# Kernel tuning notes

Hardware: AMD Instinct MI355X
Metric: run time of the kernel (lower is better)

The kernel has to match this reference:

```python
import jax, jax.numpy as jnp
import numpy as np

N_ATOMS = 20
LS_PER_ATOM = [0, 0, 1, 1, 2]   # two s, two p, one d shell per atom
N_PRIM = 8
N_COORDS = 131072


def cart_angulars(l):
    return np.array([[lx, ly, l - lx - ly]
                     for lx in range(l, -1, -1)
                     for ly in range(l - lx, -1, -1)], dtype=np.float32)


def fact2(n):
    n = int(n)
    if n <= 0:
        return 1.0
    r = 1.0
    while n > 1:
        r *= n
        n -= 2
    return r


# ---- static shell bookkeeping (grouped by angular momentum l) ----
SHELL_ATOM = np.array([a for a in range(N_ATOMS) for _ in LS_PER_ATOM])
SHELL_L = np.array([l for _ in range(N_ATOMS) for l in LS_PER_ATOM])
N_SHELLS = len(SHELL_L)
UNIQUE_LS = sorted(set(LS_PER_ATOM))

GROUPS = {}
for l in UNIQUE_LS:
    idx = np.where(SHELL_L == l)[0]
    ls = cart_angulars(l)  # [ncart, 3]
    anorms = 1.0 / np.sqrt(np.array(
        [np.prod([fact2(2 * int(e) - 1) for e in row]) for row in ls],
        dtype=np.float64))
    GROUPS[l] = (idx, ls, anorms.astype(np.float32))

NAO_CART = sum(len(GROUPS[l][1]) * len(GROUPS[l][0]) for l in UNIQUE_LS)  # 280
NAO_SPH = sum((2 * l + 1) * len(GROUPS[l][0]) for l in UNIQUE_LS)          # 260


def setup_inputs() -> dict:
    key = jax.random.key(0)
    k1, k2, k3, k4, k5, k6 = jax.random.split(key, 6)
    coords = jax.random.normal(k1, (N_COORDS, 3), dtype=jnp.float32) * 2.0
    centers = jax.random.normal(k2, (N_ATOMS, 3), dtype=jnp.float32) * 3.0
    # Gaussian exponents must be positive
    zetas = jax.random.uniform(k3, (N_SHELLS, N_PRIM), dtype=jnp.float32,
                               minval=0.2, maxval=3.0)
    coeffs = jax.random.normal(k4, (N_SHELLS, N_PRIM), dtype=jnp.float32)
    normalization = jax.random.uniform(k5, (NAO_CART,), dtype=jnp.float32,
                                       minval=0.5, maxval=1.5)
    cart2sph = jax.random.normal(k6, (NAO_CART, NAO_SPH), dtype=jnp.float32) * 0.3
    return {"coords": coords, "centers": centers, "zetas": zetas,
            "coeffs": coeffs, "normalization": normalization,
            "cart2sph": cart2sph}


def reference(coords, centers, zetas, coeffs, normalization, cart2sph):
    """Batched GTOBasis.eval_ao: [N,3] -> [N, nao_sph]."""
    n = coords.shape[0]
    pieces = []
    for l in UNIQUE_LS:
        idx, ls, anorms = GROUPS[l]
        c = centers[SHELL_ATOM[idx]]                 # [S, 3]
        rs = coords[:, None, :] - c[None]            # [N, S, 3]
        rs2 = jnp.sum(rs * rs, axis=-1)              # [N, S]
        # cartesian angular part: prod over xyz of rs**l_component
        ang = jnp.prod(rs[:, :, None, :] ** jnp.asarray(ls)[None, None],
                       axis=-1)                      # [N, S, ncart]
        ex = jnp.exp(-zetas[idx][None] * rs2[:, :, None])  # [N, S, nprim]
        rad = jnp.sum(coeffs[idx][None] * ex, axis=-1)     # [N, S]
        phis = jnp.asarray(anorms) * ang * rad[:, :, None]  # [N, S, ncart]
        pieces.append(phis.reshape(n, -1))
    aos = jnp.concatenate(pieces, axis=-1) * normalization  # [N, nao_cart]
    return jnp.dot(aos, cart2sph)                           # [N, nao_sph]
```

## Files before the change

kernel.cpp:

```cpp
#include <hip/hip_runtime.h>

typedef unsigned int uint;
typedef unsigned short ushort;
typedef __attribute__((ext_vector_type(8))) short short8;
typedef __attribute__((ext_vector_type(4))) float f32x4;
typedef __attribute__((ext_vector_type(2))) uint uint2v;

#define NSH   100
#define NPRIM 8
#define NAOC  280
#define NAOS  260
#define NATOM 20
#define KP    288
#define NKB   9
#define MT    32
#define NCOLP 272
#define BCH   (32 * NCOLP)
#define RSQRT3 0.57735026918962576f
#define LOG2E  1.4426950408889634f
#define EPS   276

#define O_RAD   0
#define O_AH    12800
#define O_AL    16896
#define O_ZETA  20992
#define O_COEF  24192
#define O_CEN   27392
#define O_CX    27712
#define O_CY    27840
#define O_CZ    27968
#define O_NORMF 28096
#define O_META  29248
#define POOLSZ  (MT * EPS * 4)

__device__ __forceinline__ ushort bf16_rne(float x) {
    uint u = __float_as_uint(x);
    return (ushort)((u + 0x7FFFu + ((u >> 16) & 1u)) >> 16);
}
__device__ __forceinline__ float bf16_to_f(ushort h) {
    return __uint_as_float(((uint)h) << 16);
}
__device__ __forceinline__ uint cvt_pk_bf16(float a, float b) {
    uint r;
    asm("v_cvt_pk_bf16_f32 %0, %1, %2" : "=v"(r) : "v"(a), "v"(b));
    return r;
}

__device__ __forceinline__ int calc_meta(int k, float& anorm) {
    int shell = 0, atom = 0, s1 = 0, s2 = 0;
    anorm = 1.0f;
    if (k < 40) {
        atom = k >> 1; shell = 5 * atom + (k & 1);
    } else if (k < 160) {
        int i = k - 40; int ip = i / 3; int c = i - 3 * ip;
        atom = ip >> 1; shell = 5 * atom + 2 + (ip & 1); s1 = 1 + c;
    } else if (k < NAOC) {
        int i = k - 160; atom = i / 6; shell = 5 * atom + 4; int c = i - 6 * atom;
        if      (c == 0) { s1 = 1; s2 = 1; }
        else if (c == 1) { s1 = 1; s2 = 2; }
        else if (c == 2) { s1 = 1; s2 = 3; }
        else if (c == 3) { s1 = 2; s2 = 2; }
        else if (c == 4) { s1 = 2; s2 = 3; }
        else             { s1 = 3; s2 = 3; }
        if (c == 0 || c == 3 || c == 5) anorm = RSQRT3;
    }
    return shell | (atom << 7) | (s1 << 12) | (s2 << 14);
}

__global__ void prep_b(const float* __restrict__ c2s, const float* __restrict__ norm,
                       ushort* __restrict__ wsHi, ushort* __restrict__ wsLo,
                       int* __restrict__ wsMeta, float* __restrict__ wsNorm) {
    if (blockIdx.x == 0) {
        for (int k = threadIdx.x; k < KP; k += 256) {
            float an;
            int m = calc_meta(k, an);
            wsMeta[k] = m;
            wsNorm[k] = (k < NAOC ? norm[k] : 0.0f) * an;
        }
    }
    int id = blockIdx.x * 256 + threadIdx.x;
    if (id >= KP * NCOLP) return;
    int k = id / NCOLP, col = id % NCOLP;
    float v = (k < NAOC && col < NAOS) ? c2s[k * NAOS + col] : 0.0f;
    ushort hi = bf16_rne(v);
    ushort lo = bf16_rne(v - bf16_to_f(hi));
    int off = (k >> 5) * BCH +
              (((col >> 4) * 4 + ((k & 31) >> 3)) * 16 + (col & 15)) * 8 + (k & 7);
    wsHi[off] = hi;
    wsLo[off] = lo;
}

template <bool USEWS>
__global__ __launch_bounds__(256, 4) void gto_mfma(
    const float* __restrict__ coords, const float* __restrict__ centers,
    const float* __restrict__ zetas, const float* __restrict__ coeffs,
    const float* __restrict__ norm, const float* __restrict__ c2s,
    const ushort* __restrict__ wsHi, const ushort* __restrict__ wsLo,
    const int* __restrict__ wsMeta, const float* __restrict__ wsNorm,
    float* __restrict__ out, int n)
{
    __shared__ __align__(16) char smem[POOLSZ];
    float*  sRad  = (float*)(smem + O_RAD);
    float*  sZeta = (float*)(smem + O_ZETA);
    float*  sCoef = (float*)(smem + O_COEF);
    float4* sCen4 = (float4*)(smem + O_CEN);
    float*  sCx   = (float*)(smem + O_CX);
    float*  sCy   = (float*)(smem + O_CY);
    float*  sCz   = (float*)(smem + O_CZ);
    float*  sNormF= (float*)(smem + O_NORMF);
    int*    sMeta = (int*)(smem + O_META);

    const int t = threadIdx.x, lane = t & 63, w = t >> 6;
    const int lr = lane & 15, lg4 = lane >> 4;
    const int P0 = blockIdx.x * MT;

    for (int i = t; i < NSH * NPRIM; i += 256) {
        sZeta[i] = zetas[i] * LOG2E;
        sCoef[i] = coeffs[i];
    }
    if (t < NATOM)
        sCen4[t] = make_float4(centers[3 * t], centers[3 * t + 1], centers[3 * t + 2], 0.0f);
    if (t < MT * 3) {
        int gi = P0 * 3 + t;
        float v = (gi < 3 * n) ? coords[gi] : 0.0f;
        int p = t / 3, c = t - 3 * (t / 3);
        if (c == 0) sCx[p] = v; else if (c == 1) sCy[p] = v; else sCz[p] = v;
    }
    if (USEWS) {
        for (int i = t; i < KP; i += 256) { sMeta[i] = wsMeta[i]; sNormF[i] = wsNorm[i]; }
    } else {
        for (int k = t; k < KP; k += 256) {
            float an;
            sMeta[k] = calc_meta(k, an);
            sNormF[k] = (k < NAOC ? norm[k] : 0.0f) * an;
        }
    }
    __syncthreads();

    #pragma unroll 1
    for (int it = 0; it < (NSH * MT + 255) / 256; ++it) {
        int id = it * 256 + t;
        if (id < NSH * MT) {
            int s = id >> 5, p = id & 31;
            int a = s / 5;
            float4 ca = sCen4[a];
            float dx = sCx[p] - ca.x;
            float dy = sCy[p] - ca.y;
            float dz = sCz[p] - ca.z;
            float r2 = dx * dx + dy * dy + dz * dz;
            float4 z0 = *(const float4*)&sZeta[s * NPRIM];
            float4 z1 = *(const float4*)&sZeta[s * NPRIM + 4];
            float4 c0 = *(const float4*)&sCoef[s * NPRIM];
            float4 c1 = *(const float4*)&sCoef[s * NPRIM + 4];
            float rad = c0.x * __builtin_amdgcn_exp2f(-z0.x * r2);
            rad += c0.y * __builtin_amdgcn_exp2f(-z0.y * r2);
            rad += c0.z * __builtin_amdgcn_exp2f(-z0.z * r2);
            rad += c0.w * __builtin_amdgcn_exp2f(-z0.w * r2);
            rad += c1.x * __builtin_amdgcn_exp2f(-z1.x * r2);
            rad += c1.y * __builtin_amdgcn_exp2f(-z1.y * r2);
            rad += c1.z * __builtin_amdgcn_exp2f(-z1.z * r2);
            rad += c1.w * __builtin_amdgcn_exp2f(-z1.w * r2);
            sRad[s * MT + p] = rad;
        }
    }

    const int pA = t & 31, kg = t >> 5;
    auto buildA = [&](int kb2) {
        const float cxp = sCx[pA], cyp = sCy[pA], czp = sCz[pA];
        const int k0 = kb2 * 32 + kg * 4;
        int4   m4  = *(const int4*)&sMeta[k0];
        float4 nf4 = *(const float4*)&sNormF[k0];
        float v[4];
        const int   mk[4] = {m4.x, m4.y, m4.z, m4.w};
        const float nf[4] = {nf4.x, nf4.y, nf4.z, nf4.w};
        #pragma unroll
        for (int j = 0; j < 4; ++j) {
            int meta = mk[j];
            int s = meta & 127, a = (meta >> 7) & 31;
            int s1 = (meta >> 12) & 3, s2 = (meta >> 14) & 3;
            float4 ca = sCen4[a];
            float dx = cxp - ca.x, dy = cyp - ca.y, dz = czp - ca.z;
            float m1 = (s1 == 0) ? 1.0f : ((s1 == 1) ? dx : ((s1 == 2) ? dy : dz));
            float m2 = (s2 == 0) ? 1.0f : ((s2 == 1) ? dx : ((s2 == 2) ? dy : dz));
            v[j] = sRad[s * MT + pA] * (m1 * m2) * nf[j];
        }
        uint h01 = cvt_pk_bf16(v[0], v[1]);
        uint h23 = cvt_pk_bf16(v[2], v[3]);
        float r0 = v[0] - __uint_as_float(h01 << 16);
        float r1 = v[1] - __uint_as_float(h01 & 0xffff0000u);
        float r2 = v[2] - __uint_as_float(h23 << 16);
        float r3 = v[3] - __uint_as_float(h23 & 0xffff0000u);
        uint l01 = cvt_pk_bf16(r0, r1);
        uint l23 = cvt_pk_bf16(r2, r3);
        const int boff = (kb2 & 1) * 2048 + ((kg >> 1) * 512 + pA * 16 + (kg & 1) * 8);
        *(uint2v*)(smem + O_AH + boff) = (uint2v){h01, h23};
        *(uint2v*)(smem + O_AL + boff) = (uint2v){l01, l23};
    };

    __syncthreads();
    buildA(0);

    f32x4 acc[5][2];
    #pragma unroll
    for (int i = 0; i < 5; ++i)
        #pragma unroll
        for (int mt = 0; mt < 2; ++mt)
            acc[i][mt] = (f32x4){0.0f, 0.0f, 0.0f, 0.0f};

    for (int kb = 0; kb < NKB; ++kb) {
        __syncthreads();

        short8 aH[2], aL[2];
        #pragma unroll
        for (int mt = 0; mt < 2; ++mt) {
            int off = (kb & 1) * 2048 + (lg4 * 32 + mt * 16 + lr) * 16;
            aH[mt] = *(const short8*)(smem + O_AH + off);
            aL[mt] = *(const short8*)(smem + O_AL + off);
        }

        if (kb + 1 < NKB) buildA(kb + 1);

        #pragma unroll
        for (int i = 0; i < 5; ++i) {
            if (i < 4 || w == 0) {
                int nt = (i == 4) ? 16 : (w * 4 + i);
                short8 bh, bl;
                if (USEWS) {
                    bh = *(const short8*)(wsHi + (size_t)kb * BCH + (nt * 64 + lane) * 8);
                    bl = *(const short8*)(wsLo + (size_t)kb * BCH + (nt * 64 + lane) * 8);
                } else {
                    #pragma unroll
                    for (int j = 0; j < 8; ++j) {
                        int k = kb * 32 + lg4 * 8 + j;
                        int col = nt * 16 + lr;
                        float v = (k < NAOC && col < NAOS) ? c2s[k * NAOS + col] : 0.0f;
                        ushort hi = bf16_rne(v);
                        bh[j] = (short)hi;
                        bl[j] = (short)bf16_rne(v - bf16_to_f(hi));
                    }
                }
                #pragma unroll
                for (int mt = 0; mt < 2; ++mt)
                    acc[i][mt] = __builtin_amdgcn_mfma_f32_16x16x32_bf16(aH[mt], bh, acc[i][mt], 0, 0, 0);
                #pragma unroll
                for (int mt = 0; mt < 2; ++mt)
                    acc[i][mt] = __builtin_amdgcn_mfma_f32_16x16x32_bf16(aH[mt], bl, acc[i][mt], 0, 0, 0);
                #pragma unroll
                for (int mt = 0; mt < 2; ++mt)
                    acc[i][mt] = __builtin_amdgcn_mfma_f32_16x16x32_bf16(aL[mt], bh, acc[i][mt], 0, 0, 0);
            }
        }
    }

    __syncthreads();
    float* ep = (float*)smem;
    #pragma unroll
    for (int i = 0; i < 5; ++i) {
        if (i < 4 || w == 0) {
            int nt = (i == 4) ? 16 : (w * 4 + i);
            int col = nt * 16 + lr;
            #pragma unroll
            for (int mt = 0; mt < 2; ++mt)
                #pragma unroll
                for (int r = 0; r < 4; ++r)
                    ep[(mt * 16 + lg4 * 4 + r) * EPS + col] = acc[i][mt][r];
        }
    }
    __syncthreads();

    for (int row = w; row < MT; row += 4) {
        int P = P0 + row;
        if (P < n)
            *(float4*)&out[(size_t)P * NAOS + lane * 4] = *(const float4*)&ep[row * EPS + lane * 4];
    }
    if (w == 1 && lane < MT) {
        int P = P0 + lane;
        if (P < n)
            *(float4*)&out[(size_t)P * NAOS + 256] = *(const float4*)&ep[lane * EPS + 256];
    }
}

extern "C" void kernel_launch(void* const* d_in, const int* in_sizes, int n_in,
                              void* d_out, int out_size, void* d_ws, size_t ws_size,
                              hipStream_t stream) {
    const float* coords  = (const float*)d_in[0];
    const float* centers = (const float*)d_in[1];
    const float* zetas   = (const float*)d_in[2];
    const float* coeffs  = (const float*)d_in[3];
    const float* norm    = (const float*)d_in[4];
    const float* c2s     = (const float*)d_in[5];
    float* out = (float*)d_out;
    int n = in_sizes[0] / 3;
    int grid = (n + MT - 1) / MT;

    ushort* wsHi = (ushort*)d_ws;
    ushort* wsLo = wsHi + (size_t)KP * NCOLP;
    int*    wsMeta = (int*)(wsLo + (size_t)KP * NCOLP);
    float*  wsNorm = (float*)(wsMeta + KP);
    const size_t WS_NEED = (size_t)2 * KP * NCOLP * sizeof(ushort) + KP * 8;

    if (ws_size >= WS_NEED) {
        prep_b<<<(KP * NCOLP + 255) / 256, 256, 0, stream>>>(c2s, norm, wsHi, wsLo, wsMeta, wsNorm);
        gto_mfma<true><<<grid, 256, 0, stream>>>(coords, centers, zetas, coeffs, norm, c2s,
                                                 wsHi, wsLo, wsMeta, wsNorm, out, n);
    } else {
        gto_mfma<false><<<grid, 256, 0, stream>>>(coords, centers, zetas, coeffs, norm, c2s,
                                                  nullptr, nullptr, nullptr, nullptr, out, n);
    }
}
```

Measured before the change: 105.6 us.

## Build MFMA A fragments in registers instead of double-buffered shared memory

After: 155.1 us. 46.9% more time.

```diff
diff --git a/kernel.cpp b/kernel.cpp
--- a/kernel.cpp
+++ b/kernel.cpp
@@ -4,7 +4,6 @@
 typedef unsigned short ushort;
 typedef __attribute__((ext_vector_type(8))) short short8;
 typedef __attribute__((ext_vector_type(4))) float f32x4;
-typedef __attribute__((ext_vector_type(2))) uint uint2v;
 
 #define NSH   100
 #define NPRIM 8
@@ -19,18 +18,17 @@
 #define RSQRT3 0.57735026918962576f
 #define LOG2E  1.4426950408889634f
 #define EPS   276
+#define RSTRIDE 33
 
 #define O_RAD   0
-#define O_AH    12800
-#define O_AL    16896
-#define O_ZETA  20992
-#define O_COEF  24192
-#define O_CEN   27392
-#define O_CX    27712
-#define O_CY    27840
-#define O_CZ    27968
-#define O_NORMF 28096
-#define O_META  29248
+#define O_ZETA  13200
+#define O_COEF  16400
+#define O_CEN   19600
+#define O_CX    19920
+#define O_CY    20048
+#define O_CZ    20176
+#define O_NORMF 20304
+#define O_META  21456
 #define POOLSZ  (MT * EPS * 4)
 
 __device__ __forceinline__ ushort bf16_rne(float x) {
@@ -160,45 +158,13 @@
             rad += c1.y * __builtin_amdgcn_exp2f(-z1.y * r2);
             rad += c1.z * __builtin_amdgcn_exp2f(-z1.z * r2);
             rad += c1.w * __builtin_amdgcn_exp2f(-z1.w * r2);
-            sRad[s * MT + p] = rad;
-        }
-    }
-
-    const int pA = t & 31, kg = t >> 5;
-    auto buildA = [&](int kb2) {
-        const float cxp = sCx[pA], cyp = sCy[pA], czp = sCz[pA];
-        const int k0 = kb2 * 32 + kg * 4;
-        int4   m4  = *(const int4*)&sMeta[k0];
-        float4 nf4 = *(const float4*)&sNormF[k0];
-        float v[4];
-        const int   mk[4] = {m4.x, m4.y, m4.z, m4.w};
-        const float nf[4] = {nf4.x, nf4.y, nf4.z, nf4.w};
-        #pragma unroll
-        for (int j = 0; j < 4; ++j) {
-            int meta = mk[j];
-            int s = meta & 127, a = (meta >> 7) & 31;
-            int s1 = (meta >> 12) & 3, s2 = (meta >> 14) & 3;
-            float4 ca = sCen4[a];
-            float dx = cxp - ca.x, dy = cyp - ca.y, dz = czp - ca.z;
-            float m1 = (s1 == 0) ? 1.0f : ((s1 == 1) ? dx : ((s1 == 2) ? dy : dz));
-            float m2 = (s2 == 0) ? 1.0f : ((s2 == 1) ? dx : ((s2 == 2) ? dy : dz));
-            v[j] = sRad[s * MT + pA] * (m1 * m2) * nf[j];
-        }
-        uint h01 = cvt_pk_bf16(v[0], v[1]);
-        uint h23 = cvt_pk_bf16(v[2], v[3]);
-        float r0 = v[0] - __uint_as_float(h01 << 16);
-        float r1 = v[1] - __uint_as_float(h01 & 0xffff0000u);
-        float r2 = v[2] - __uint_as_float(h23 << 16);
-        float r3 = v[3] - __uint_as_float(h23 & 0xffff0000u);
-        uint l01 = cvt_pk_bf16(r0, r1);
-        uint l23 = cvt_pk_bf16(r2, r3);
-        const int boff = (kb2 & 1) * 2048 + ((kg >> 1) * 512 + pA * 16 + (kg & 1) * 8);
-        *(uint2v*)(smem + O_AH + boff) = (uint2v){h01, h23};
-        *(uint2v*)(smem + O_AL + boff) = (uint2v){l01, l23};
-    };
-
+            sRad[s * RSTRIDE + p] = rad;
+        }
+    }
     __syncthreads();
-    buildA(0);
+
+    const float cx0 = sCx[lr],      cy0 = sCy[lr],      cz0 = sCz[lr];
+    const float cx1 = sCx[16 + lr], cy1 = sCy[16 + lr], cz1 = sCz[16 + lr];
 
     f32x4 acc[5][2];
     #pragma unroll
@@ -207,18 +173,50 @@
         for (int mt = 0; mt < 2; ++mt)
             acc[i][mt] = (f32x4){0.0f, 0.0f, 0.0f, 0.0f};
 
+    union U4 { uint u[4]; short8 s; };
+
+    #pragma unroll 1
     for (int kb = 0; kb < NKB; ++kb) {
-        __syncthreads();
+        const int k0 = kb * 32 + lg4 * 8;
+        int4   m4a = *(const int4*)&sMeta[k0];
+        int4   m4b = *(const int4*)&sMeta[k0 + 4];
+        float4 n4a = *(const float4*)&sNormF[k0];
+        float4 n4b = *(const float4*)&sNormF[k0 + 4];
+        const int   mk[8] = {m4a.x, m4a.y, m4a.z, m4a.w, m4b.x, m4b.y, m4b.z, m4b.w};
+        const float nf[8] = {n4a.x, n4a.y, n4a.z, n4a.w, n4b.x, n4b.y, n4b.z, n4b.w};
 
         short8 aH[2], aL[2];
         #pragma unroll
         for (int mt = 0; mt < 2; ++mt) {
-            int off = (kb & 1) * 2048 + (lg4 * 32 + mt * 16 + lr) * 16;
-            aH[mt] = *(const short8*)(smem + O_AH + off);
-            aL[mt] = *(const short8*)(smem + O_AL + off);
-        }
-
-        if (kb + 1 < NKB) buildA(kb + 1);
+            const float cxp = mt ? cx1 : cx0;
+            const float cyp = mt ? cy1 : cy0;
+            const float czp = mt ? cz1 : cz0;
+            const int   p   = mt * 16 + lr;
+            U4 uh, ul;
+            #pragma unroll
+            for (int jp = 0; jp < 4; ++jp) {
+                float v2[2];
+                #pragma unroll
+                for (int h = 0; h < 2; ++h) {
+                    const int j = jp * 2 + h;
+                    int meta = mk[j];
+                    int s = meta & 127, a = (meta >> 7) & 31;
+                    int s1 = (meta >> 12) & 3, s2 = (meta >> 14) & 3;
+                    float4 ca = sCen4[a];
+                    float dx = cxp - ca.x, dy = cyp - ca.y, dz = czp - ca.z;
+                    float m1 = (s1 == 0) ? 1.0f : ((s1 == 1) ? dx : ((s1 == 2) ? dy : dz));
+                    float m2 = (s2 == 0) ? 1.0f : ((s2 == 1) ? dx : ((s2 == 2) ? dy : dz));
+                    v2[h] = sRad[s * RSTRIDE + p] * (m1 * m2) * nf[j];
+                }
+                uint hp = cvt_pk_bf16(v2[0], v2[1]);
+                float r0 = v2[0] - __uint_as_float(hp << 16);
+                float r1 = v2[1] - __uint_as_float(hp & 0xffff0000u);
+                uh.u[jp] = hp;
+                ul.u[jp] = cvt_pk_bf16(r0, r1);
+            }
+            aH[mt] = uh.s;
+            aL[mt] = ul.s;
+        }
 
         #pragma unroll
         for (int i = 0; i < 5; ++i) {
```

## Double point tile to 64 with 512-thread blocks for B-fragment reuse

Applied to the files above, without the earlier changes.

New measurement: 246.9 us. +133.8%, slower.

```diff
diff --git a/kernel.cpp b/kernel.cpp
--- a/kernel.cpp
+++ b/kernel.cpp
@@ -4,7 +4,6 @@
 typedef unsigned short ushort;
 typedef __attribute__((ext_vector_type(8))) short short8;
 typedef __attribute__((ext_vector_type(4))) float f32x4;
-typedef __attribute__((ext_vector_type(2))) uint uint2v;
 
 #define NSH   100
 #define NPRIM 8
@@ -13,7 +12,8 @@
 #define NATOM 20
 #define KP    288
 #define NKB   9
-#define MT    32
+#define MT    64
+#define NTHR  512
 #define NCOLP 272
 #define BCH   (32 * NCOLP)
 #define RSQRT3 0.57735026918962576f
@@ -21,17 +21,17 @@
 #define EPS   276
 
 #define O_RAD   0
-#define O_AH    12800
-#define O_AL    16896
-#define O_ZETA  20992
-#define O_COEF  24192
-#define O_CEN   27392
-#define O_CX    27712
-#define O_CY    27840
-#define O_CZ    27968
-#define O_NORMF 28096
-#define O_META  29248
-#define POOLSZ  (MT * EPS * 4)
+#define O_AH    25600
+#define O_AL    33792
+#define O_ZETA  41984
+#define O_COEF  45184
+#define O_CEN   48384
+#define O_CX    48704
+#define O_CY    48960
+#define O_CZ    49216
+#define O_NORMF 49472
+#define O_META  50624
+#define POOLSZ  51776
 
 __device__ __forceinline__ ushort bf16_rne(float x) {
     uint u = __float_as_uint(x);
@@ -91,7 +91,7 @@
 }
 
 template <bool USEWS>
-__global__ __launch_bounds__(256, 4) void gto_mfma(
+__global__ __launch_bounds__(NTHR, 4) void gto_mfma(
     const float* __restrict__ coords, const float* __restrict__ centers,
     const float* __restrict__ zetas, const float* __restrict__ coeffs,
     const float* __restrict__ norm, const float* __restrict__ c2s,
@@ -114,7 +114,7 @@
     const int lr = lane & 15, lg4 = lane >> 4;
     const int P0 = blockIdx.x * MT;
 
-    for (int i = t; i < NSH * NPRIM; i += 256) {
+    for (int i = t; i < NSH * NPRIM; i += NTHR) {
         sZeta[i] = zetas[i] * LOG2E;
         sCoef[i] = coeffs[i];
     }
@@ -127,9 +127,9 @@
         if (c == 0) sCx[p] = v; else if (c == 1) sCy[p] = v; else sCz[p] = v;
     }
     if (USEWS) {
-        for (int i = t; i < KP; i += 256) { sMeta[i] = wsMeta[i]; sNormF[i] = wsNorm[i]; }
+        for (int i = t; i < KP; i += NTHR) { sMeta[i] = wsMeta[i]; sNormF[i] = wsNorm[i]; }
     } else {
-        for (int k = t; k < KP; k += 256) {
+        for (int k = t; k < KP; k += NTHR) {
             float an;
             sMeta[k] = calc_meta(k, an);
             sNormF[k] = (k < NAOC ? norm[k] : 0.0f) * an;
@@ -138,10 +138,10 @@
     __syncthreads();
 
     #pragma unroll 1
-    for (int it = 0; it < (NSH * MT + 255) / 256; ++it) {
-        int id = it * 256 + t;
+    for (int it = 0; it < (NSH * MT + NTHR - 1) / NTHR; ++it) {
+        int id = it * NTHR + t;
         if (id < NSH * MT) {
-            int s = id >> 5, p = id & 31;
+            int s = id >> 6, p = id & 63;
             int a = s / 5;
             float4 ca = sCen4[a];
             float dx = sCx[p] - ca.x;
@@ -164,15 +164,15 @@
         }
     }
 
-    const int pA = t & 31, kg = t >> 5;
+    const int pA = t & 63, q = t >> 6;
     auto buildA = [&](int kb2) {
         const float cxp = sCx[pA], cyp = sCy[pA], czp = sCz[pA];
-        const int k0 = kb2 * 32 + kg * 4;
+        const int k0 = kb2 * 32 + q * 4;
         int4   m4  = *(const int4*)&sMeta[k0];
         float4 nf4 = *(const float4*)&sNormF[k0];
-        float v[4];
         const int   mk[4] = {m4.x, m4.y, m4.z, m4.w};
         const float nf[4] = {nf4.x, nf4.y, nf4.z, nf4.w};
+        float v[4];
         #pragma unroll
         for (int j = 0; j < 4; ++j) {
             int meta = mk[j];
@@ -181,8 +181,8 @@
             float4 ca = sCen4[a];
             float dx = cxp - ca.x, dy = cyp - ca.y, dz = czp - ca.z;
             float m1 = (s1 == 0) ? 1.0f : ((s1 == 1) ? dx : ((s1 == 2) ? dy : dz));
-            float m2 = (s2 == 0) ? 1.0f : ((s2 == 1) ? dx : ((s2 == 2) ? dy : dz));
-            v[j] = sRad[s * MT + pA] * (m1 * m2) * nf[j];
+            float m2v = (s2 == 0) ? 1.0f : ((s2 == 1) ? dx : ((s2 == 2) ? dy : dz));
+            v[j] = sRad[s * MT + pA] * (m1 * m2v) * nf[j];
         }
         uint h01 = cvt_pk_bf16(v[0], v[1]);
         uint h23 = cvt_pk_bf16(v[2], v[3]);
@@ -192,43 +192,51 @@
         float r3 = v[3] - __uint_as_float(h23 & 0xffff0000u);
         uint l01 = cvt_pk_bf16(r0, r1);
         uint l23 = cvt_pk_bf16(r2, r3);
-        const int boff = (kb2 & 1) * 2048 + ((kg >> 1) * 512 + pA * 16 + (kg & 1) * 8);
-        *(uint2v*)(smem + O_AH + boff) = (uint2v){h01, h23};
-        *(uint2v*)(smem + O_AL + boff) = (uint2v){l01, l23};
+        const int boff = (kb2 & 1) * 4096 + (q >> 1) * 1024 + pA * 16 + (q & 1) * 8;
+        *(uint2*)(smem + O_AH + boff) = make_uint2(h01, h23);
+        *(uint2*)(smem + O_AL + boff) = make_uint2(l01, l23);
     };
 
     __syncthreads();
     buildA(0);
 
-    f32x4 acc[5][2];
+    const ushort* pH  = wsHi + (2 * w * 64 + lane) * 8;
+    const ushort* pL  = wsLo + (2 * w * 64 + lane) * 8;
+    const ushort* pH2 = wsHi + (16 * 64 + lane) * 8;
+    const ushort* pL2 = wsLo + (16 * 64 + lane) * 8;
+
+    f32x4 acc[3][4];
     #pragma unroll
-    for (int i = 0; i < 5; ++i)
-        #pragma unroll
-        for (int mt = 0; mt < 2; ++mt)
-            acc[i][mt] = (f32x4){0.0f, 0.0f, 0.0f, 0.0f};
-
+    for (int ti = 0; ti < 3; ++ti)
+        #pragma unroll
+        for (int m = 0; m < 4; ++m)
+            acc[ti][m] = (f32x4){0.0f, 0.0f, 0.0f, 0.0f};
+
+    #pragma unroll 1
     for (int kb = 0; kb < NKB; ++kb) {
         __syncthreads();
 
-        short8 aH[2], aL[2];
-        #pragma unroll
-        for (int mt = 0; mt < 2; ++mt) {
-            int off = (kb & 1) * 2048 + (lg4 * 32 + mt * 16 + lr) * 16;
-            aH[mt] = *(const short8*)(smem + O_AH + off);
-            aL[mt] = *(const short8*)(smem + O_AL + off);
+        const int base = (kb & 1) * 4096;
+        short8 aH[4], aL[4];
+        #pragma unroll
+        for (int m = 0; m < 4; ++m) {
+            const int off = base + lg4 * 1024 + (m * 16 + lr) * 16;
+            aH[m] = *(const short8*)(smem + O_AH + off);
+            aL[m] = *(const short8*)(smem + O_AL + off);
         }
 
         if (kb + 1 < NKB) buildA(kb + 1);
 
         #pragma unroll
-        for (int i = 0; i < 5; ++i) {
-            if (i < 4 || w == 0) {
-                int nt = (i == 4) ? 16 : (w * 4 + i);
+        for (int ti = 0; ti < 3; ++ti) {
+            if (ti < 2 || w == 0) {
                 short8 bh, bl;
                 if (USEWS) {
-                    bh = *(const short8*)(wsHi + (size_t)kb * BCH + (nt * 64 + lane) * 8);
-                    bl = *(const short8*)(wsLo + (size_t)kb * BCH + (nt * 64 + lane) * 8);
+                    if (ti == 0)      { bh = *(const short8*)pH;          bl = *(const short8*)pL; }
+                    else if (ti == 1) { bh = *(const short8*)(pH + 512);  bl = *(const short8*)(pL + 512); }
+                    else              { bh = *(const short8*)pH2;         bl = *(const short8*)pL2; }
                 } else {
+                    int nt = (ti == 2) ? 16 : (2 * w + ti);
                     #pragma unroll
                     for (int j = 0; j < 8; ++j) {
                         int k = kb * 32 + lg4 * 8 + j;
@@ -240,43 +248,46 @@
                     }
                 }
                 #pragma unroll
-                for (int mt = 0; mt < 2; ++mt)
-                    acc[i][mt] = __builtin_amdgcn_mfma_f32_16x16x32_bf16(aH[mt], bh, acc[i][mt], 0, 0, 0);
+                for (int m = 0; m < 4; ++m)
+                    acc[ti][m] = __builtin_amdgcn_mfma_f32_16x16x32_bf16(aH[m], bh, acc[ti][m], 0, 0, 0);
                 #pragma unroll
-                for (int mt = 0; mt < 2; ++mt)
-                    acc[i][mt] = __builtin_amdgcn_mfma_f32_16x16x32_bf16(aH[mt], bl, acc[i][mt], 0, 0, 0);
+                for (int m = 0; m < 4; ++m)
+                    acc[ti][m] = __builtin_amdgcn_mfma_f32_16x16x32_bf16(aH[m], bl, acc[ti][m], 0, 0, 0);
                 #pragma unroll
-                for (int mt = 0; mt < 2; ++mt)
-                    acc[i][mt] = __builtin_amdgcn_mfma_f32_16x16x32_bf16(aL[mt], bh, acc[i][mt], 0, 0, 0);
+                for (int m = 0; m < 4; ++m)
+                    acc[ti][m] = __builtin_amdgcn_mfma_f32_16x16x32_bf16(aL[m], bh, acc[ti][m], 0, 0, 0);
             }
         }
-    }
-
-    __syncthreads();
+        pH += BCH; pL += BCH; pH2 += BCH; pL2 += BCH;
+    }
+
     float* ep = (float*)smem;
-    #pragma unroll
-    for (int i = 0; i < 5; ++i) {
-        if (i < 4 || w == 0) {
-            int nt = (i == 4) ? 16 : (w * 4 + i);
-            int col = nt * 16 + lr;
-            #pragma unroll
-            for (int mt = 0; mt < 2; ++mt)
+    #pragma unroll 1
+    for (int qm = 0; qm < 4; ++qm) {
+        __syncthreads();
+        #pragma unroll
+        for (int ti = 0; ti < 3; ++ti) {
+            if (ti < 2 || w == 0) {
+                int nt = (ti == 2) ? 16 : (2 * w + ti);
+                int col = nt * 16 + lr;
                 #pragma unroll
                 for (int r = 0; r < 4; ++r)
-                    ep[(mt * 16 + lg4 * 4 + r) * EPS + col] = acc[i][mt][r];
-        }
-    }
-    __syncthreads();
-
-    for (int row = w; row < MT; row += 4) {
-        int P = P0 + row;
-        if (P < n)
-            *(float4*)&out[(size_t)P * NAOS + lane * 4] = *(const float4*)&ep[row * EPS + lane * 4];
-    }
-    if (w == 1 && lane < MT) {
-        int P = P0 + lane;
-        if (P < n)
-            *(float4*)&out[(size_t)P * NAOS + 256] = *(const float4*)&ep[lane * EPS + 256];
+                    ep[(lg4 * 4 + r) * EPS + col] = acc[ti][qm][r];
+            }
+        }
+        __syncthreads();
+        const int row = t >> 5;
+        const int c   = t & 31;
+        const int P   = P0 + qm * 16 + row;
+        if (P < n) {
+            #pragma unroll
+            for (int c4 = 0; c4 < 3; ++c4) {
+                int col4 = c + c4 * 32;
+                if (col4 < 65)
+                    *(float4*)&out[(size_t)P * NAOS + col4 * 4] =
+                        *(const float4*)&ep[row * EPS + col4 * 4];
+            }
+        }
     }
 }
 
@@ -301,10 +312,10 @@
 
     if (ws_size >= WS_NEED) {
         prep_b<<<(KP * NCOLP + 255) / 256, 256, 0, stream>>>(c2s, norm, wsHi, wsLo, wsMeta, wsNorm);
-        gto_mfma<true><<<grid, 256, 0, stream>>>(coords, centers, zetas, coeffs, norm, c2s,
-                                                 wsHi, wsLo, wsMeta, wsNorm, out, n);
+        gto_mfma<true><<<grid, NTHR, 0, stream>>>(coords, centers, zetas, coeffs, norm, c2s,
+                                                  wsHi, wsLo, wsMeta, wsNorm, out, n);
     } else {
-        gto_mfma<false><<<grid, 256, 0, stream>>>(coords, centers, zetas, coeffs, norm, c2s,
-                                                  nullptr, nullptr, nullptr, nullptr, out, n);
-    }
-}
+        gto_mfma<false><<<grid, NTHR, 0, stream>>>(coords, centers, zetas, coeffs, norm, c2s,
+                                                   nullptr, nullptr, nullptr, nullptr, out, n);
+    }
+}
```
